# Kernel tuning notes

Hardware: AMD Instinct MI355X
Metric: run time of the kernel (lower is better)

The kernel has to match this reference:

```python
import jax, jax.numpy as jnp
import numpy as np

N_HEADS = 16

def _rotate_half(t):
    # t: [B, H, T, hs]; split last dim in half, return cat(-x2, x1)
    hs = t.shape[-1]
    x1, x2 = t[..., : hs // 2], t[..., hs // 2 :]
    return jnp.concatenate((-x2, x1), axis=-1)

def _rope_pos(T, hs, dtype):
    inv_freq = 1.0 / (10000.0 ** (jnp.arange(0, hs, 2, dtype=jnp.float32) / hs))
    freqs = jnp.arange(T, dtype=jnp.float32)[:, None] * inv_freq[None, :]  # [T, hs/2]
    pos = jnp.concatenate((freqs, freqs), axis=-1)  # [T, hs]
    return pos

def setup_inputs() -> dict:
    key = jax.random.key(0)
    ks = jax.random.split(key, 5)
    d = 2048
    x = jax.random.normal(ks[0], (2, 2048, d), dtype=jnp.float32)
    W_attn = jax.random.normal(ks[1], (d, 3 * d), dtype=jnp.float32) * (1.0 / np.sqrt(d))
    b_attn = jax.random.normal(ks[2], (3 * d,), dtype=jnp.float32) * 0.02
    W_proj = jax.random.normal(ks[3], (d, d), dtype=jnp.float32) * (1.0 / np.sqrt(d))
    b_proj = jax.random.normal(ks[4], (d,), dtype=jnp.float32) * 0.02
    return {"x": x, "W_attn": W_attn, "b_attn": b_attn, "W_proj": W_proj, "b_proj": b_proj}

def reference(x, W_attn, b_attn, W_proj, b_proj):
    B, T, C = x.shape
    nh = N_HEADS
    hs = C // nh
    qkv = x @ W_attn + b_attn  # [B, T, 3C]
    q, k, v = jnp.split(qkv, 3, axis=-1)
    # [B, T, C] -> [B, nh, T, hs]
    def to_heads(t):
        return t.reshape(B, T, nh, hs).transpose(0, 2, 1, 3)
    q, k, v = to_heads(q), to_heads(k), to_heads(v)
    # RoPE
    pos = _rope_pos(T, hs, x.dtype)  # [T, hs]
    cos, sin = jnp.cos(pos).astype(x.dtype), jnp.sin(pos).astype(x.dtype)
    q = q * cos + _rotate_half(q) * sin
    k = k * cos + _rotate_half(k) * sin
    # causal SDPA
    scale = 1.0 / np.sqrt(hs)
    scores = jnp.einsum('bhqd,bhkd->bhqk', q, k) * scale  # [B, nh, T, T]
    causal = jnp.tril(jnp.ones((T, T), dtype=bool))
    scores = jnp.where(causal, scores, jnp.finfo(scores.dtype).min)
    att = jax.nn.softmax(scores, axis=-1)
    out = jnp.einsum('bhqk,bhkd->bhqd', att, v)  # [B, nh, T, hs]
    y = out.transpose(0, 2, 1, 3).reshape(B, T, C)
    return y @ W_proj + b_proj
```

## Files before the change

kernel.cpp:

```cpp
#include <hip/hip_runtime.h>
#include <stdint.h>

typedef unsigned short u16;
typedef __attribute__((ext_vector_type(8))) short short8;
typedef __attribute__((ext_vector_type(4))) float f32x4;
typedef __attribute__((ext_vector_type(4))) unsigned short u16x4;

#define DEV __device__ __forceinline__

DEV u16 f2bf(float f) {
  union { float f; unsigned u; } v; v.f = f;
  unsigned r = v.u + 0x7fffu + ((v.u >> 16) & 1u);
  return (u16)(r >> 16);
}
DEV float bf2f(u16 b) {
  union { unsigned u; float f; } v; v.u = ((unsigned)b) << 16;
  return v.f;
}
DEV void gload_lds16(const void* g, void* l) {
  __builtin_amdgcn_global_load_lds((const __attribute__((address_space(1))) void*)g,
                                   (__attribute__((address_space(3))) void*)l,
                                   16, 0, 0);
}
DEV void block_barrier() {
  asm volatile("" ::: "memory");
  __builtin_amdgcn_s_barrier();
  asm volatile("" ::: "memory");
}

__global__ void k_conv(const float* __restrict__ in, u16* __restrict__ out, int n4) {
  int i = blockIdx.x * blockDim.x + threadIdx.x;
  if (i >= n4) return;
  const f32x4 v = *(const f32x4*)(in + (size_t)i * 4);
  u16x4 o;
  o[0] = f2bf(v[0]); o[1] = f2bf(v[1]); o[2] = f2bf(v[2]); o[3] = f2bf(v[3]);
  *(u16x4*)(out + (size_t)i * 4) = o;
}

__global__ void k_tconv(const float* __restrict__ in, u16* __restrict__ out, int R, int C) {
  __shared__ float tile[32][33];
  int c0 = blockIdx.x * 32, r0 = blockIdx.y * 32;
  int tx = threadIdx.x, ty = threadIdx.y;
#pragma unroll
  for (int j = 0; j < 32; j += 8)
    tile[ty + j][tx] = in[(size_t)(r0 + ty + j) * C + (c0 + tx)];
  __syncthreads();
#pragma unroll
  for (int j = 0; j < 32; j += 8)
    out[(size_t)(c0 + ty + j) * R + (r0 + tx)] = f2bf(tile[tx][ty + j]);
}

__global__ __launch_bounds__(512, 2) void k_gemmqkv(const u16* __restrict__ A,
                                                    const u16* __restrict__ Bt,
                                                    const float* __restrict__ bias,
                                                    u16* __restrict__ qh,
                                                    u16* __restrict__ kh,
                                                    u16* __restrict__ vt) {
  const int Kld = 2048, nt = 32;
  __shared__ __align__(16) short smem[4][256 * 64];
  const int tid = threadIdx.x;
  const int wid = tid >> 6, lane = tid & 63;
  const int gx = gridDim.x;
  const int nwg = gx * gridDim.y;
  const int orig = blockIdx.y * gx + blockIdx.x;
  const int lg = (orig & 7) * (nwg >> 3) + (orig >> 3);
  const int bm = (lg % gx) * 256, bn = (lg / gx) * 256;
  const int wr = wid >> 2, wc = wid & 3;
  const int r = lane & 15, kq = lane >> 4, r7 = lane & 7;

  int aoff[4], boff[4], lbase[4];
#pragma unroll
  for (int j = 0; j < 4; ++j) {
    int c = j * 512 + wid * 64 + lane;
    int row = c >> 3, ch = c & 7;
    aoff[j] = (bm + row) * Kld + (ch ^ (row & 7)) * 8;
    boff[j] = (bn + row) * Kld + (ch ^ (row & 7)) * 8;
    lbase[j] = (j * 512 + wid * 64) * 16;
  }

#define STG_A(k0, buf, j) gload_lds16(A + aoff[j] + (k0), (char*)&smem[(buf)][0] + lbase[j])
#define STG_B(k0, buf, j) gload_lds16(Bt + boff[j] + (k0), (char*)&smem[2 + (buf)][0] + lbase[j])
#define RD_A(AF, MH, KK)                                                        \
  _Pragma("unroll")                                                             \
  for (int m2 = 0; m2 < 4; ++m2)                                                \
    AF[m2] = *(const short8*)&As[(wr * 128 + (MH) * 64 + m2 * 16 + r) * 64      \
                                 + (((KK) * 4 + kq) ^ r7) * 8];
#define RD_B(KK)                                                                \
  _Pragma("unroll")                                                             \
  for (int nf = 0; nf < 4; ++nf)                                                \
    bfr[KK][nf] = *(const short8*)&Bs[(wc * 64 + nf * 16 + r) * 64              \
                                      + (((KK) * 4 + kq) ^ r7) * 8];
#define PH_MFMA(AF, MH, KK)                                                     \
  __builtin_amdgcn_s_setprio(1);                                                \
  _Pragma("unroll")                                                             \
  for (int m2 = 0; m2 < 4; ++m2)                                                \
    _Pragma("unroll")                                                           \
    for (int nf = 0; nf < 4; ++nf)                                              \
      acc[(MH) * 4 + m2][nf] = __builtin_amdgcn_mfma_f32_16x16x32_bf16(         \
          AF[m2], bfr[KK][nf], acc[(MH) * 4 + m2][nf], 0, 0, 0);                \
  __builtin_amdgcn_s_setprio(0);

  f32x4 acc[8][4];
  const f32x4 zero = {0.f, 0.f, 0.f, 0.f};
#pragma unroll
  for (int i = 0; i < 8; ++i)
#pragma unroll
    for (int j = 0; j < 4; ++j) acc[i][j] = zero;

#pragma unroll
  for (int j = 0; j < 4; ++j) STG_A(0, 0, j);
#pragma unroll
  for (int j = 0; j < 4; ++j) STG_B(0, 0, j);
#pragma unroll
  for (int j = 0; j < 4; ++j) STG_B(64, 1, j);
  asm volatile("s_waitcnt vmcnt(4)" ::: "memory");
  block_barrier();

#pragma unroll 1
  for (int t = 0; t < nt; ++t) {
    const int cur = t & 1, nxt = cur ^ 1;
    const short* As = &smem[cur][0];
    const short* Bs = &smem[2 + cur][0];
    const int kA = (t + 1) * 64, kB = (t + 2) * 64;
    const bool sA = (t + 1 < nt), sB = (t + 2 < nt);
    short8 bfr[2][4];
    short8 af[4];

    RD_B(0)
    RD_A(af, 0, 0)
    if (sA) { STG_A(kA, nxt, 0); STG_A(kA, nxt, 1); }
    block_barrier();
    PH_MFMA(af, 0, 0)
    block_barrier();

    RD_B(1)
    RD_A(af, 0, 1)
    if (sA) { STG_A(kA, nxt, 2); STG_A(kA, nxt, 3); }
    block_barrier();
    PH_MFMA(af, 0, 1)
    block_barrier();

    RD_A(af, 1, 0)
    if (sB) { STG_B(kB, cur, 0); STG_B(kB, cur, 1); }
    block_barrier();
    PH_MFMA(af, 1, 0)
    block_barrier();

    RD_A(af, 1, 1)
    if (sB) { STG_B(kB, cur, 2); STG_B(kB, cur, 3); }
    block_barrier();
    PH_MFMA(af, 1, 1)
    if (t + 1 < nt) {
      if (sB) asm volatile("s_waitcnt vmcnt(4)" ::: "memory");
      else    asm volatile("s_waitcnt vmcnt(0)" ::: "memory");
    }
    block_barrier();
  }
#undef STG_A
#undef STG_B
#undef RD_A
#undef RD_B
#undef PH_MFMA

  const int by = lg / gx;
  const int part = by >> 3;
  const int b_ = bm >> 11;
  const int tb = bm & 2047;
  const int hbase = (bn & 2047) >> 7;
  u16* ob = (u16*)&smem[0][0];

#pragma unroll
  for (int nf = 0; nf < 4; ++nf) {
    int nl = wc * 64 + nf * 16 + r;
    float bv = bias[bn + nl];
#pragma unroll
    for (int mf = 0; mf < 8; ++mf) {
      int mlb = wr * 128 + mf * 16 + kq * 4;
#pragma unroll
      for (int i = 0; i < 4; ++i) {
        int ml = mlb + i;
        int cl = (part == 2)
          ? (nl ^ (((ml >> 2) & 3) << 4) ^ (((ml >> 4) & 7) << 1))
          : (nl ^ (((ml >> 2) & 3) << 4));
        ob[ml * 256 + cl] = f2bf(acc[mf][nf][i] + bv);
      }
    }
  }
  block_barrier();

  if (part == 2) {
#pragma unroll 1
    for (int iter = 0; iter < 32; ++iter) {
      int dl = iter * 8 + wid;
      int hh = hbase + (dl >> 7), d = dl & 127;
      int tl4 = lane * 4;
      int cl = dl ^ ((lane & 3) << 4) ^ (((lane >> 2) & 7) << 1);
      u16x4 o;
#pragma unroll
      for (int j = 0; j < 4; ++j) o[j] = ob[(tl4 + j) * 256 + cl];
      *(u16x4*)(vt + ((size_t)(b_ * 16 + hh) * 128 + d) * 2048 + tb + tl4) = o;
    }
  } else {
    u16* dst = part ? kh : qh;
    const int nl2 = lane * 4;
    const int hh = hbase + (nl2 >> 7);
    const int d0 = nl2 & 127;
    const int hi = (nl2 >> 6) & 1;
    float inv0 = exp2f((float)(nl2 & 63) * -0.20762050593045077f);
    const float k1 = 0.8659643233600653f;
    float invj[4];
    invj[0] = inv0; invj[1] = inv0 * k1; invj[2] = invj[1] * k1; invj[3] = invj[2] * k1;
#pragma unroll 1
    for (int iter = 0; iter < 32; ++iter) {
      int tl = iter * 8 + wid;
      float tg = (float)(tb + tl);
      int xr = ((tl >> 2) & 3) << 4;
      int base = tl * 256 + (nl2 ^ xr);
      int pbase = tl * 256 + ((nl2 ^ 64) ^ xr);
      u16x4 o;
#pragma unroll
      for (int j = 0; j < 4; ++j) {
        float vo = bf2f(ob[base + j]);
        float vp = bf2f(ob[pbase + j]);
        float sn, cs;
        sincosf(tg * invj[j], &sn, &cs);
        float vr = hi ? (vo * cs + vp * sn) : (vo * cs - vp * sn);
        o[j] = f2bf(vr);
      }
      *(u16x4*)(dst + ((size_t)(b_ * 16 + hh) * 2048 + (tb + tl)) * 128 + d0) = o;
    }
  }
}

template <bool OUT_BF16, bool SPLITK>
__global__ __launch_bounds__(512, 2) void k_gemm3(const u16* __restrict__ A,
                                                  const u16* __restrict__ Bt,
                                                  const float* __restrict__ bias,
                                                  void* __restrict__ Cv,
                                                  int M, int N, int Kld, int nkt) {
  __shared__ __align__(16) short lA[2][256 * 64];
  __shared__ __align__(16) short lB[2][256 * 64];
  const int tid = threadIdx.x;
  const int wid = tid >> 6, lane = tid & 63;
  const int gx = gridDim.x;
  const int nwg = gx * gridDim.y;
  const int orig = blockIdx.y * gx + blockIdx.x;
  const int lg = (orig & 7) * (nwg >> 3) + (orig >> 3);
  const int bm = (lg % gx) * 256, bn = (lg / gx) * 256;
  const int wr = wid >> 2, wc = wid & 3;
  const int r = lane & 15, kq = lane >> 4, r7 = lane & 7;
  const int kz = SPLITK ? blockIdx.z * (nkt << 6) : 0;

  int aoff[4], boff[4], lbase[4];
#pragma unroll
  for (int j = 0; j < 4; ++j) {
    int c = j * 512 + wid * 64 + lane;
    int row = c >> 3, ch = c & 7;
    aoff[j] = (bm + row) * Kld + kz + (ch ^ (row & 7)) * 8;
    boff[j] = (bn + row) * Kld + kz + (ch ^ (row & 7)) * 8;
    lbase[j] = (j * 512 + wid * 64) * 16;
  }

#define STG_A(k0, buf, j) gload_lds16(A + aoff[j] + (k0), (char*)&lA[(buf)][0] + lbase[j])
#define STG_B(k0, buf, j) gload_lds16(Bt + boff[j] + (k0), (char*)&lB[(buf)][0] + lbase[j])
#define RD_A(AF, MH, KK)                                                        \
  _Pragma("unroll")                                                             \
  for (int m2 = 0; m2 < 4; ++m2)                                                \
    AF[m2] = *(const short8*)&As[(wr * 128 + (MH) * 64 + m2 * 16 + r) * 64      \
                                 + (((KK) * 4 + kq) ^ r7) * 8];
#define RD_B(KK)                                                                \
  _Pragma("unroll")                                                             \
  for (int nf = 0; nf < 4; ++nf)                                                \
    bfr[KK][nf] = *(const short8*)&Bs[(wc * 64 + nf * 16 + r) * 64              \
                                      + (((KK) * 4 + kq) ^ r7) * 8];
#define PH_MFMA(AF, MH, KK)                                                     \
  __builtin_amdgcn_s_setprio(1);                                                \
  _Pragma("unroll")                                                             \
  for (int m2 = 0; m2 < 4; ++m2)                                                \
    _Pragma("unroll")                                                           \
    for (int nf = 0; nf < 4; ++nf)                                              \
      acc[(MH) * 4 + m2][nf] = __builtin_amdgcn_mfma_f32_16x16x32_bf16(         \
          AF[m2], bfr[KK][nf], acc[(MH) * 4 + m2][nf], 0, 0, 0);                \
  __builtin_amdgcn_s_setprio(0);

  f32x4 acc[8][4];
  const f32x4 zero = {0.f, 0.f, 0.f, 0.f};
#pragma unroll
  for (int i = 0; i < 8; ++i)
#pragma unroll
    for (int j = 0; j < 4; ++j) acc[i][j] = zero;

  const int nt = nkt;

#pragma unroll
  for (int j = 0; j < 4; ++j) STG_A(0, 0, j);
#pragma unroll
  for (int j = 0; j < 4; ++j) STG_B(0, 0, j);
  if (nt > 1) {
#pragma unroll
    for (int j = 0; j < 4; ++j) STG_B(64, 1, j);
    asm volatile("s_waitcnt vmcnt(4)" ::: "memory");
  } else {
    asm volatile("s_waitcnt vmcnt(0)" ::: "memory");
  }
  block_barrier();

#pragma unroll 1
  for (int t = 0; t < nt; ++t) {
    const int cur = t & 1, nxt = cur ^ 1;
    const short* As = &lA[cur][0];
    const short* Bs = &lB[cur][0];
    const int kA = (t + 1) * 64, kB = (t + 2) * 64;
    const bool sA = (t + 1 < nt), sB = (t + 2 < nt);
    short8 bfr[2][4];
    short8 af[4];

    RD_B(0)
    RD_A(af, 0, 0)
    if (sA) { STG_A(kA, nxt, 0); STG_A(kA, nxt, 1); }
    block_barrier();
    PH_MFMA(af, 0, 0)
    block_barrier();

    RD_B(1)
    RD_A(af, 0, 1)
    if (sA) { STG_A(kA, nxt, 2); STG_A(kA, nxt, 3); }
    block_barrier();
    PH_MFMA(af, 0, 1)
    block_barrier();

    RD_A(af, 1, 0)
    if (sB) { STG_B(kB, cur, 0); STG_B(kB, cur, 1); }
    block_barrier();
    PH_MFMA(af, 1, 0)
    block_barrier();

    RD_A(af, 1, 1)
    if (sB) { STG_B(kB, cur, 2); STG_B(kB, cur, 3); }
    block_barrier();
    PH_MFMA(af, 1, 1)
    if (t + 1 < nt) {
      if (sB) asm volatile("s_waitcnt vmcnt(4)" ::: "memory");
      else    asm volatile("s_waitcnt vmcnt(0)" ::: "memory");
    }
    block_barrier();
  }
#undef STG_A
#undef STG_B
#undef RD_A
#undef RD_B
#undef PH_MFMA

#pragma unroll
  for (int mf = 0; mf < 8; ++mf)
#pragma unroll
    for (int nf = 0; nf < 4; ++nf) {
      int n = bn + wc * 64 + nf * 16 + r;
      float bv = SPLITK ? 0.f : bias[n];
#pragma unroll
      for (int i = 0; i < 4; ++i) {
        int m = bm + wr * 128 + mf * 16 + kq * 4 + i;
        float val = acc[mf][nf][i] + bv;
        if (SPLITK)
          ((float*)Cv)[(size_t)blockIdx.z * M * N + (size_t)m * N + n] = val;
        else if (OUT_BF16)
          ((u16*)Cv)[(size_t)m * N + n] = f2bf(val);
        else
          ((float*)Cv)[(size_t)m * N + n] = val;
      }
    }
}

__global__ void k_fadd(const float* __restrict__ p, const float* __restrict__ bias,
                       float* __restrict__ y, int n4) {
  const int half4 = 2097152;
  for (int i = blockIdx.x * blockDim.x + threadIdx.x; i < n4; i += gridDim.x * blockDim.x) {
    f32x4 a = *(const f32x4*)(p + (size_t)i * 4);
    f32x4 b = *(const f32x4*)(p + (size_t)(i + half4) * 4);
    f32x4 bv = *(const f32x4*)(bias + ((i & 511) << 2));
    f32x4 o = a + b + bv;
    *(f32x4*)(y + (size_t)i * 4) = o;
  }
}

__global__ __launch_bounds__(256) void k_attn(const u16* __restrict__ qh,
                                              const u16* __restrict__ kh,
                                              const u16* __restrict__ vt,
                                              u16* __restrict__ out) {
  __shared__ __align__(16) short lK[2][64 * 128];
  __shared__ __align__(16) short lV[2][128 * 64];
  __shared__ __align__(16) short lP[64 * 64];
  const int tid = threadIdx.x, wid = tid >> 6, lane = tid & 63;
  const int p = blockIdx.x, h = blockIdx.y, b = blockIdx.z;
  const size_t bh = (size_t)b * 16 + h;
  const u16* qb = qh + bh * 2048 * 128;
  const u16* kb = kh + bh * 2048 * 128;
  const u16* vb = vt + bh * 128 * 2048;
  const int r = lane & 15, kq = lane >> 4;
  const int r7 = r & 7;
  const int wrow = wid * 16;
  const float scale2 = 0.08838834764831845f * 1.4426950408889634f;

  int koff[4], voff[4];
#pragma unroll
  for (int i = 0; i < 4; ++i) {
    int ci = (wid * 4 + i) * 64 + lane;
    int krow = ci >> 4, kch = ci & 15;
    koff[i] = krow * 128 + ((kch ^ (krow & 7)) * 8);
    int vrow = ci >> 3, vch = ci & 7;
    voff[i] = vrow * 2048 + ((vch ^ (vrow & 7)) * 8);
  }

#pragma unroll 1
  for (int seg = 0; seg < 2; ++seg) {
    const int j = seg ? 31 - p : p;
    const int q0 = j * 64;
    const int nkt = j + 1;

    short8 qa[4];
#pragma unroll
    for (int kk = 0; kk < 4; ++kk)
      qa[kk] = *(const short8*)(qb + (size_t)(q0 + wrow + r) * 128 + kk * 32 + kq * 8);

    f32x4 O[8];
    const f32x4 zero = {0.f, 0.f, 0.f, 0.f};
#pragma unroll
    for (int nf = 0; nf < 8; ++nf) O[nf] = zero;
    float lp[4] = {0.f, 0.f, 0.f, 0.f};

#pragma unroll
    for (int i = 0; i < 4; ++i) {
      gload_lds16(kb + koff[i], (char*)&lK[0][0] + (wid * 4 + i) * 1024);
      gload_lds16(vb + voff[i], (char*)&lV[0][0] + (wid * 4 + i) * 1024);
    }

#pragma unroll 1
    for (int kt = 0; kt < nkt; ++kt) {
      const int cur = kt & 1;
      if (kt + 1 < nkt) {
        const size_t kbase = (size_t)(kt + 1) * 8192, vbase = (size_t)(kt + 1) * 64;
#pragma unroll
        for (int i = 0; i < 4; ++i) {
          gload_lds16(kb + kbase + koff[i], (char*)&lK[cur ^ 1][0] + (wid * 4 + i) * 1024);
          gload_lds16(vb + vbase + voff[i], (char*)&lV[cur ^ 1][0] + (wid * 4 + i) * 1024);
        }
        asm volatile("s_waitcnt vmcnt(8)" ::: "memory");
      } else {
        asm volatile("s_waitcnt vmcnt(0)" ::: "memory");
      }
      block_barrier();

      f32x4 S[4];
#pragma unroll
      for (int nf = 0; nf < 4; ++nf) S[nf] = zero;
#pragma unroll
      for (int kk = 0; kk < 4; ++kk) {
        short8 kf[4];
#pragma unroll
        for (int nf = 0; nf < 4; ++nf)
          kf[nf] = *(const short8*)&lK[cur][(nf * 16 + r) * 128 + ((kk * 4 + kq) ^ r7) * 8];
#pragma unroll
        for (int nf = 0; nf < 4; ++nf)
          S[nf] = __builtin_amdgcn_mfma_f32_16x16x32_bf16(qa[kk], kf[nf], S[nf], 0, 0, 0);
      }

      const bool diag = (kt == nkt - 1);
#pragma unroll
      for (int nf = 0; nf < 4; ++nf)
#pragma unroll
        for (int i = 0; i < 4; ++i) {
          float pv = exp2f(S[nf][i] * scale2);
          if (diag) {
            int kg = kt * 64 + nf * 16 + r;
            int qg = q0 + wrow + kq * 4 + i;
            pv = (kg > qg) ? 0.f : pv;
          }
          lp[i] += pv;
          int row = wrow + kq * 4 + i;
          int cl = (nf * 2 + (r >> 3)) ^ ((kq * 4 + i) & 7);
          lP[row * 64 + cl * 8 + r7] = (short)f2bf(pv);
        }

#pragma unroll
      for (int kk = 0; kk < 2; ++kk) {
        short8 pa = *(const short8*)&lP[(wrow + r) * 64 + ((kk * 4 + kq) ^ r7) * 8];
#pragma unroll
        for (int nf = 0; nf < 8; ++nf) {
          short8 vf = *(const short8*)&lV[cur][(nf * 16 + r) * 64 + ((kk * 4 + kq) ^ r7) * 8];
          O[nf] = __builtin_amdgcn_mfma_f32_16x16x32_bf16(pa, vf, O[nf], 0, 0, 0);
        }
      }
      asm volatile("s_waitcnt lgkmcnt(0)" ::: "memory");
      block_barrier();
    }

    float inv[4];
#pragma unroll
    for (int i = 0; i < 4; ++i) {
      float v = lp[i];
      v += __shfl_xor(v, 1);
      v += __shfl_xor(v, 2);
      v += __shfl_xor(v, 4);
      v += __shfl_xor(v, 8);
      inv[i] = 1.f / v;
    }
#pragma unroll
    for (int nf = 0; nf < 8; ++nf)
#pragma unroll
      for (int i = 0; i < 4; ++i) {
        int qg = q0 + wrow + kq * 4 + i;
        out[(size_t)(b * 2048 + qg) * 2048 + h * 128 + nf * 16 + r] = f2bf(O[nf][i] * inv[i]);
      }
  }
}

extern "C" void kernel_launch(void* const* d_in, const int* in_sizes, int n_in,
                              void* d_out, int out_size, void* d_ws, size_t ws_size,
                              hipStream_t stream) {
  const float* x      = (const float*)d_in[0];
  const float* W_attn = (const float*)d_in[1];
  const float* b_attn = (const float*)d_in[2];
  const float* W_proj = (const float*)d_in[3];
  const float* b_proj = (const float*)d_in[4];
  float* y = (float*)d_out;

  u16* xb     = (u16*)d_ws;
  u16* wqkvT  = xb     + (size_t)4096 * 2048;
  u16* wprojT = wqkvT  + (size_t)6144 * 2048;
  u16* qkv    = wprojT + (size_t)2048 * 2048;
  u16* qh     = qkv    + (size_t)4096 * 6144;
  u16* kh     = qh     + (size_t)4096 * 2048;
  u16* vt     = kh     + (size_t)4096 * 2048;
  u16* attout = vt     + (size_t)4096 * 2048;
  if (ws_size < (size_t)83886080 * 2) return;

  float* pproj = (float*)qkv;

  k_conv<<<8192, 256, 0, stream>>>(x, xb, 2097152);
  k_tconv<<<dim3(192, 64), dim3(32, 8), 0, stream>>>(W_attn, wqkvT, 2048, 6144);
  k_tconv<<<dim3(64, 64), dim3(32, 8), 0, stream>>>(W_proj, wprojT, 2048, 2048);
  k_gemmqkv<<<dim3(16, 24), 512, 0, stream>>>(xb, wqkvT, b_attn, qh, kh, vt);
  k_attn<<<dim3(16, 16, 2), 256, 0, stream>>>(qh, kh, vt, attout);
  k_gemm3<false, true><<<dim3(16, 8, 2), 512, 0, stream>>>(attout, wprojT, b_proj, pproj, 4096, 2048, 2048, 16);
  k_fadd<<<2048, 256, 0, stream>>>(pproj, b_proj, y, 2097152);
}
```

Baseline: 321.0 us.

## Load V fragments directly from global, drop V LDS buffer, prescale Q

Removes the V double buffer in LDS and has each wave load its V^T MFMA fragments straight from global memory into registers every key tile. This halves LDS use, so a second workgroup can fit per CU, which launch bounds of 2 now request. The softmax scale and log2e factor are folded into Q during the RoPE stage so the attention kernel skips one multiply per score. The direct global loads are issued after the barrier and are not prefetched, so their latency may be exposed, and register pressure rises with 16 short8 values held per lane.

Result: slower. 371.1 us (+15.6%).

```diff
diff --git a/kernel.cpp b/kernel.cpp
--- a/kernel.cpp
+++ b/kernel.cpp
@@ -202,6 +202,7 @@
     }
   } else {
     u16* dst = part ? kh : qh;
+    const float qscale = part ? 1.0f : 0.12751744766834352f;
     const int nl2 = lane * 4;
     const int hh = hbase + (nl2 >> 7);
     const int d0 = nl2 & 127;
@@ -225,7 +226,7 @@
         float sn, cs;
         sincosf(tg * invj[j], &sn, &cs);
         float vr = hi ? (vo * cs + vp * sn) : (vo * cs - vp * sn);
-        o[j] = f2bf(vr);
+        o[j] = f2bf(vr * qscale);
       }
       *(u16x4*)(dst + ((size_t)(b_ * 16 + hh) * 2048 + (tb + tl)) * 128 + d0) = o;
     }
@@ -383,12 +384,11 @@
   }
 }
 
-__global__ __launch_bounds__(256) void k_attn(const u16* __restrict__ qh,
-                                              const u16* __restrict__ kh,
-                                              const u16* __restrict__ vt,
-                                              u16* __restrict__ out) {
+__global__ __launch_bounds__(256, 2) void k_attn(const u16* __restrict__ qh,
+                                                 const u16* __restrict__ kh,
+                                                 const u16* __restrict__ vt,
+                                                 u16* __restrict__ out) {
   __shared__ __align__(16) short lK[2][64 * 128];
-  __shared__ __align__(16) short lV[2][128 * 64];
   __shared__ __align__(16) short lP[64 * 64];
   const int tid = threadIdx.x, wid = tid >> 6, lane = tid & 63;
   const int p = blockIdx.x, h = blockIdx.y, b = blockIdx.z;
@@ -399,16 +399,13 @@
   const int r = lane & 15, kq = lane >> 4;
   const int r7 = r & 7;
   const int wrow = wid * 16;
-  const float scale2 = 0.08838834764831845f * 1.4426950408889634f;
-
-  int koff[4], voff[4];
+
+  int koff[4];
 #pragma unroll
   for (int i = 0; i < 4; ++i) {
     int ci = (wid * 4 + i) * 64 + lane;
     int krow = ci >> 4, kch = ci & 15;
     koff[i] = krow * 128 + ((kch ^ (krow & 7)) * 8);
-    int vrow = ci >> 3, vch = ci & 7;
-    voff[i] = vrow * 2048 + ((vch ^ (vrow & 7)) * 8);
   }
 
 #pragma unroll 1
@@ -429,27 +426,31 @@
     float lp[4] = {0.f, 0.f, 0.f, 0.f};
 
 #pragma unroll
-    for (int i = 0; i < 4; ++i) {
+    for (int i = 0; i < 4; ++i)
       gload_lds16(kb + koff[i], (char*)&lK[0][0] + (wid * 4 + i) * 1024);
-      gload_lds16(vb + voff[i], (char*)&lV[0][0] + (wid * 4 + i) * 1024);
-    }
 
 #pragma unroll 1
     for (int kt = 0; kt < nkt; ++kt) {
       const int cur = kt & 1;
+      const int kt0 = kt * 64;
       if (kt + 1 < nkt) {
-        const size_t kbase = (size_t)(kt + 1) * 8192, vbase = (size_t)(kt + 1) * 64;
-#pragma unroll
-        for (int i = 0; i < 4; ++i) {
+        const size_t kbase = (size_t)(kt + 1) * 8192;
+#pragma unroll
+        for (int i = 0; i < 4; ++i)
           gload_lds16(kb + kbase + koff[i], (char*)&lK[cur ^ 1][0] + (wid * 4 + i) * 1024);
-          gload_lds16(vb + vbase + voff[i], (char*)&lV[cur ^ 1][0] + (wid * 4 + i) * 1024);
-        }
-        asm volatile("s_waitcnt vmcnt(8)" ::: "memory");
+        asm volatile("s_waitcnt vmcnt(4)" ::: "memory");
       } else {
         asm volatile("s_waitcnt vmcnt(0)" ::: "memory");
       }
       block_barrier();
 
+      short8 vf[8][2];
+#pragma unroll
+      for (int nf = 0; nf < 8; ++nf)
+#pragma unroll
+        for (int kk = 0; kk < 2; ++kk)
+          vf[nf][kk] = *(const short8*)(vb + (size_t)(nf * 16 + r) * 2048 + kt0 + kk * 32 + kq * 8);
+
       f32x4 S[4];
 #pragma unroll
       for (int nf = 0; nf < 4; ++nf) S[nf] = zero;
@@ -469,9 +470,9 @@
       for (int nf = 0; nf < 4; ++nf)
 #pragma unroll
         for (int i = 0; i < 4; ++i) {
-          float pv = exp2f(S[nf][i] * scale2);
+          float pv = exp2f(S[nf][i]);
           if (diag) {
-            int kg = kt * 64 + nf * 16 + r;
+            int kg = kt0 + nf * 16 + r;
             int qg = q0 + wrow + kq * 4 + i;
             pv = (kg > qg) ? 0.f : pv;
           }
@@ -485,10 +486,8 @@
       for (int kk = 0; kk < 2; ++kk) {
         short8 pa = *(const short8*)&lP[(wrow + r) * 64 + ((kk * 4 + kq) ^ r7) * 8];
 #pragma unroll
-        for (int nf = 0; nf < 8; ++nf) {
-          short8 vf = *(const short8*)&lV[cur][(nf * 16 + r) * 64 + ((kk * 4 + kq) ^ r7) * 8];
-          O[nf] = __builtin_amdgcn_mfma_f32_16x16x32_bf16(pa, vf, O[nf], 0, 0, 0);
-        }
+        for (int nf = 0; nf < 8; ++nf)
+          O[nf] = __builtin_amdgcn_mfma_f32_16x16x32_bf16(pa, vf[nf][kk], O[nf], 0, 0, 0);
       }
       asm volatile("s_waitcnt lgkmcnt(0)" ::: "memory");
       block_barrier();
```
